# Optimization experiments

Measured on AMD Instinct MI355X. Metric: run time of the kernel, lower is better.

Reference implementation:

```python
import jax, jax.numpy as jnp
import numpy as np

N_NODES = 10000
N_EDGES = 80000
N_GRAPHS = 64
HEADS = 8
F_IN = 128
D1, D2, D3 = 512, 256, 128  # per-head (and output, concat=False) widths
OUT_DIM = 10


def _lin(key, fin, fout):
    kw, kb = jax.random.split(key)
    w = jax.random.normal(kw, (fin, fout), dtype=jnp.float32) * 0.05
    b = jax.random.normal(kb, (fout,), dtype=jnp.float32) * 0.05
    return w, b


def setup_inputs() -> dict:
    key = jax.random.key(0)
    ks = jax.random.split(key, 24)
    x = jax.random.normal(ks[0], (N_NODES, F_IN), dtype=jnp.float32)
    edge_index = jax.random.randint(ks[1], (2, N_EDGES), 0, N_NODES, dtype=jnp.int64)
    batch = jnp.sort(jax.random.randint(ks[2], (N_NODES,), 0, N_GRAPHS, dtype=jnp.int64))
    d = {"x": x, "edge_index": edge_index, "batch": batch}
    # conv1: 128 -> heads*512 (q,k,v), skip 128 -> 512
    d["w_q1"], d["b_q1"] = _lin(ks[3], F_IN, HEADS * D1)
    d["w_k1"], d["b_k1"] = _lin(ks[4], F_IN, HEADS * D1)
    d["w_v1"], d["b_v1"] = _lin(ks[5], F_IN, HEADS * D1)
    d["w_s1"], d["b_s1"] = _lin(ks[6], F_IN, D1)
    # conv2: 512 -> heads*256, skip 512 -> 256
    d["w_q2"], d["b_q2"] = _lin(ks[7], D1, HEADS * D2)
    d["w_k2"], d["b_k2"] = _lin(ks[8], D1, HEADS * D2)
    d["w_v2"], d["b_v2"] = _lin(ks[9], D1, HEADS * D2)
    d["w_s2"], d["b_s2"] = _lin(ks[10], D1, D2)
    # conv3: 256 -> heads*128, skip 256 -> 128
    d["w_q3"], d["b_q3"] = _lin(ks[11], D2, HEADS * D3)
    d["w_k3"], d["b_k3"] = _lin(ks[12], D2, HEADS * D3)
    d["w_v3"], d["b_v3"] = _lin(ks[13], D2, HEADS * D3)
    d["w_s3"], d["b_s3"] = _lin(ks[14], D2, D3)
    # global attention gate + final fc
    d["w_g"], d["b_g"] = _lin(ks[15], D3, 1)
    d["w_fc"], d["b_fc"] = _lin(ks[16], D3, OUT_DIM)
    return d


def _seg_softmax(a, seg, n):
    m = jax.ops.segment_max(a, seg, num_segments=n)
    e = jnp.exp(a - m[seg])
    s = jax.ops.segment_sum(e, seg, num_segments=n)
    return e / (s[seg] + 1e-16)


def _tconv(x, edge_index, wq, bq, wk, bk, wv, bv, ws, bs):
    # PyG TransformerConv, concat=False, root_weight=True, no edge features
    n = x.shape[0]
    c = wq.shape[1] // HEADS
    q = (x @ wq + bq).reshape(n, HEADS, c)
    k = (x @ wk + bk).reshape(n, HEADS, c)
    v = (x @ wv + bv).reshape(n, HEADS, c)
    src, dst = edge_index[0], edge_index[1]
    a = jnp.einsum('ehc,ehc->eh', q[dst], k[src]) / jnp.sqrt(jnp.float32(c))
    alpha = _seg_softmax(a, dst, n)                                  # [E, H]
    out = jax.ops.segment_sum(v[src] * alpha[..., None], dst, num_segments=n)
    return out.mean(axis=1) + (x @ ws + bs)                          # mean over heads + skip


def reference(x, edge_index, batch,
              w_q1, b_q1, w_k1, b_k1, w_v1, b_v1, w_s1, b_s1,
              w_q2, b_q2, w_k2, b_k2, w_v2, b_v2, w_s2, b_s2,
              w_q3, b_q3, w_k3, b_k3, w_v3, b_v3, w_s3, b_s3,
              w_g, b_g, w_fc, b_fc):
    h = jax.nn.elu(_tconv(x, edge_index, w_q1, b_q1, w_k1, b_k1, w_v1, b_v1, w_s1, b_s1))
    h = jax.nn.elu(_tconv(h, edge_index, w_q2, b_q2, w_k2, b_k2, w_v2, b_v2, w_s2, b_s2))
    h = jax.nn.elu(_tconv(h, edge_index, w_q3, b_q3, w_k3, b_k3, w_v3, b_v3, w_s3, b_s3))
    # GlobalAttention pooling: softmax(gate) over nodes within each graph
    gate = h @ w_g + b_g                                             # [N, 1]
    gate = _seg_softmax(gate, batch, N_GRAPHS)
    g = jax.ops.segment_sum(gate * h, batch, num_segments=N_GRAPHS)  # [G, D3]
    return g @ w_fc + b_fc                                           # [G, OUT_DIM]
```

## Files before the change

### kernel.cpp

```cpp
#include <hip/hip_runtime.h>
#include <math.h>

typedef __bf16 bf16;
typedef __bf16 bf16x8 __attribute__((ext_vector_type(8)));
typedef __bf16 bf16x4 __attribute__((ext_vector_type(4)));
typedef __bf16 bf16x2 __attribute__((ext_vector_type(2)));
typedef float f32x4 __attribute__((ext_vector_type(4)));
typedef float f32x2 __attribute__((ext_vector_type(2)));
typedef unsigned int u32;

#define N_NODES 10000
#define N_EDGES 80000
#define N_GRAPHS 64

template<int EPL> struct VecT;
template<> struct VecT<8>{ typedef bf16x8 type; };
template<> struct VecT<4>{ typedef bf16x4 type; };
template<> struct VecT<2>{ typedef bf16x2 type; };

__device__ inline unsigned f2ord(float f){
  unsigned u = __float_as_uint(f);
  return (u & 0x80000000u) ? ~u : (u | 0x80000000u);
}
__device__ inline float ord2f(unsigned u){
  return (u & 0x80000000u) ? __uint_as_float(u & 0x7fffffffu) : __uint_as_float(~u);
}

__device__ inline void gload_lds16(const bf16* g, bf16* l){
  __builtin_amdgcn_global_load_lds(
      (const __attribute__((address_space(1))) unsigned int*)g,
      (__attribute__((address_space(3))) unsigned int*)l, 16, 0, 0);
}

__global__ __launch_bounds__(256) void detect_f32_k(const unsigned short* __restrict__ raw, int n,
                                                    int* __restrict__ flagF){
  int i = blockIdx.x*256 + threadIdx.x;
  if (i < n){
    unsigned e = (raw[i] >> 7) & 0xFFu;
    if (e >= 0xC0u) atomicOr(flagF, 1);
  }
}

struct CvPack {
  const void* src[11];
  bf16* dst[11];
  int pre[12];
  int rl[11];
  int st[11];
};
__global__ __launch_bounds__(256) void convert_all(CvPack p, const int* __restrict__ flagF){
  int gid = blockIdx.x*256 + threadIdx.x;
  if (gid >= p.pre[11]) return;
  int t = 0;
  while (gid >= p.pre[t+1]) ++t;
  int i = gid - p.pre[t];
  bool f = (*flagF != 0);
  float v = f ? ((const float*)p.src[t])[i] : (float)((const bf16*)p.src[t])[i];
  int row = i / p.rl[t], col = i - row*p.rl[t];
  p.dst[t][(size_t)row*p.st[t] + col] = (bf16)v;
}

__global__ __launch_bounds__(256) void detect_i64(const int* __restrict__ raw, int* __restrict__ flag){
  int i = blockIdx.x*256 + threadIdx.x;
  if (i < 4000 && raw[2*i+1] != 0) atomicOr(flag, 1);
}

__global__ __launch_bounds__(256) void conv_idx(const int* __restrict__ ei_raw,
                                                const int* __restrict__ b_raw,
                                                const int* __restrict__ flag,
                                                int* __restrict__ src, int* __restrict__ dst,
                                                int* __restrict__ bat, int* __restrict__ cnt){
  int i = blockIdx.x*256 + threadIdx.x;
  bool i32 = (*flag != 0);
  if (i < N_EDGES){
    int s = i32 ? ei_raw[i]   : ei_raw[2*i];
    int d = i32 ? ei_raw[N_EDGES + i] : ei_raw[2*(N_EDGES + i)];
    s = min(max(s, 0), N_NODES-1);
    d = min(max(d, 0), N_NODES-1);
    src[i] = s; dst[i] = d;
    atomicAdd(&cnt[d], 1);
  }
  if (i < N_NODES){
    int b = i32 ? b_raw[i] : b_raw[2*i];
    bat[i] = min(max(b, 0), N_GRAPHS-1);
  }
}

__global__ __launch_bounds__(256) void scanA(const int* __restrict__ cnt, int* __restrict__ fill,
                                             int* __restrict__ bsum, int N){
  __shared__ int s[256];
  int i = blockIdx.x*256 + threadIdx.x;
  int v = (i < N) ? cnt[i] : 0;
  s[threadIdx.x] = v;
  __syncthreads();
  for (int d = 1; d < 256; d <<= 1){
    int t = (threadIdx.x >= d) ? s[threadIdx.x - d] : 0;
    __syncthreads();
    s[threadIdx.x] += t;
    __syncthreads();
  }
  if (i < N) fill[i] = s[threadIdx.x] - v;
  if (threadIdx.x == 255) bsum[blockIdx.x] = s[255];
}
__global__ __launch_bounds__(64) void scanB(int* __restrict__ bsum, int nb){
  if (threadIdx.x == 0){
    int a = 0;
    for (int b = 0; b < nb; ++b){ int t = bsum[b]; bsum[b] = a; a += t; }
  }
}
__global__ __launch_bounds__(256) void scanC(const int* __restrict__ bsum, int* __restrict__ fill,
                                             int* __restrict__ row_ptr, int N){
  int i = blockIdx.x*256 + threadIdx.x;
  if (i < N){
    int st = fill[i] + bsum[i >> 8];
    fill[i] = st;
    row_ptr[i] = st;
  }
  if (i == 0) row_ptr[N] = N_EDGES;
}

__global__ __launch_bounds__(256) void fill_csr(const int* __restrict__ dst,
                                                int* __restrict__ fill, int* __restrict__ eids){
  int e = blockIdx.x*256 + threadIdx.x;
  if (e < N_EDGES){
    int p = atomicAdd(&fill[dst[e]], 1);
    eids[p] = e;
  }
}

__global__ __launch_bounds__(256)
void gemm_bias(const bf16* __restrict__ A, int lda,
               const bf16* __restrict__ Bt,
               const bf16* __restrict__ bias, bf16* __restrict__ Cout, int ldc,
               int M, int N, int K)
{
  __shared__ bf16 As[128*64];
  __shared__ bf16 Bs[128*64];
  const int tid = threadIdx.x;
  const int lane = tid & 63;
  const int wave = tid >> 6;
  const int m0 = blockIdx.y * 128, n0 = blockIdx.x * 128;
  const int wm = (wave >> 1) * 64, wn = (wave & 1) * 64;
  const int l15 = lane & 15, l4 = lane >> 4;
  const int srow = lane >> 3;
  const int schunk = lane & 7;

  f32x4 acc[4][4] = {};

  for (int k0 = 0; k0 < K; k0 += 64){
    #pragma unroll
    for (int j = 0; j < 4; ++j){
      int r0 = (wave*4 + j)*8;
      int r  = r0 + srow;
      int gc = schunk ^ (r & 7);
      int ga = m0 + r; if (ga >= M) ga = M-1;
      gload_lds16(A  + (size_t)ga*lda      + k0 + gc*8, As + r0*64);
      gload_lds16(Bt + (size_t)(n0 + r)*K  + k0 + gc*8, Bs + r0*64);
    }
    __syncthreads();
    #pragma unroll
    for (int kt = 0; kt < 2; ++kt){
      bf16x8 af[4], bfr[4];
      #pragma unroll
      for (int mt = 0; mt < 4; ++mt){
        int row = wm + mt*16 + l15;
        int p = (kt*4 + l4) ^ (l15 & 7);
        af[mt] = *(const bf16x8*)(As + row*64 + p*8);
      }
      #pragma unroll
      for (int nt = 0; nt < 4; ++nt){
        int row = wn + nt*16 + l15;
        int p = (kt*4 + l4) ^ (l15 & 7);
        bfr[nt] = *(const bf16x8*)(Bs + row*64 + p*8);
      }
      #pragma unroll
      for (int mt = 0; mt < 4; ++mt)
        #pragma unroll
        for (int nt = 0; nt < 4; ++nt)
          acc[mt][nt] = __builtin_amdgcn_mfma_f32_16x16x32_bf16(af[mt], bfr[nt], acc[mt][nt], 0, 0, 0);
    }
    __syncthreads();
  }

  #pragma unroll
  for (int nt = 0; nt < 4; ++nt){
    int col = n0 + wn + nt*16 + l15;
    float bv = (float)bias[col];
    #pragma unroll
    for (int mt = 0; mt < 4; ++mt){
      int rbase = m0 + wm + mt*16 + l4*4;
      #pragma unroll
      for (int r = 0; r < 4; ++r){
        int row = rbase + r;
        if (row < M) Cout[(size_t)row*ldc + col] = (bf16)(acc[mt][nt][r] + bv);
      }
    }
  }
}

__global__ __launch_bounds__(512, 1)
void gemm8p_bias(const bf16* __restrict__ A, int lda,
                 const bf16* __restrict__ Bt,
                 const bf16* __restrict__ bias, bf16* __restrict__ Cout, int ldc,
                 int M, int K)
{
  __shared__ bf16 As[3][256*64];
  __shared__ bf16 Bs[3][128*64];
  const int tid = threadIdx.x;
  const int lane = tid & 63;
  const int wave = tid >> 6;
  const int m0 = blockIdx.y * 256, n0 = blockIdx.x * 128;
  const int wm = (wave >> 1) * 64;
  const int wn = (wave & 1) * 64;
  const int l15 = lane & 15, l4 = lane >> 4;
  const int srow = lane >> 3;
  const int schunk = lane & 7;
  const int NT = K >> 6;

  auto stageA = [&](int t, int j){
    int b = t % 3;
    int r0 = (wave + j*8)*8;
    int r  = r0 + srow;
    int gc = schunk ^ srow;
    int ga = m0 + r; if (ga >= M) ga = M-1;
    gload_lds16(A + (size_t)ga*lda + t*64 + gc*8, &As[b][r0*64]);
  };
  auto stageB = [&](int t, int j){
    int b = t % 3;
    int r0 = (wave + j*8)*8;
    int r  = r0 + srow;
    int gc = schunk ^ srow;
    gload_lds16(Bt + (size_t)(n0 + r)*K + t*64 + gc*8, &Bs[b][r0*64]);
  };

  stageA(0,0); stageA(0,1); stageA(0,2); stageA(0,3); stageB(0,0); stageB(0,1);
  if (NT > 1){ stageA(1,0); stageA(1,1); stageA(1,2); stageA(1,3); stageB(1,0); stageB(1,1); }
  if (NT > 1) asm volatile("s_waitcnt vmcnt(6)" ::: "memory");
  else        asm volatile("s_waitcnt vmcnt(0)" ::: "memory");
  __builtin_amdgcn_s_barrier();

  f32x4 acc[4][4] = {};

  for (int t = 0; t < NT; ++t){
    const bf16* as = &As[t % 3][0];
    const bf16* bs = &Bs[t % 3][0];
    bf16x8 bfr[4][2];
    bf16x8 af[2][2];

    #pragma unroll
    for (int nt2 = 0; nt2 < 4; ++nt2)
      #pragma unroll
      for (int kt = 0; kt < 2; ++kt){
        int row = wn + nt2*16 + l15;
        int p = (kt*4 + l4) ^ (l15 & 7);
        bfr[nt2][kt] = *(const bf16x8*)(bs + row*64 + p*8);
      }
    #pragma unroll
    for (int i = 0; i < 2; ++i)
      #pragma unroll
      for (int kt = 0; kt < 2; ++kt){
        int row = wm + i*16 + l15;
        int p = (kt*4 + l4) ^ (l15 & 7);
        af[i][kt] = *(const bf16x8*)(as + row*64 + p*8);
      }
    if (t + 2 < NT){ stageA(t+2,0); stageA(t+2,1); stageB(t+2,0); }
    __builtin_amdgcn_s_setprio(1);
    #pragma unroll
    for (int i = 0; i < 2; ++i)
      #pragma unroll
      for (int nt2 = 0; nt2 < 4; ++nt2)
        #pragma unroll
        for (int kt = 0; kt < 2; ++kt)
          acc[i][nt2] = __builtin_amdgcn_mfma_f32_16x16x32_bf16(af[i][kt], bfr[nt2][kt], acc[i][nt2], 0, 0, 0);
    __builtin_amdgcn_s_setprio(0);

    #pragma unroll
    for (int i = 0; i < 2; ++i)
      #pragma unroll
      for (int kt = 0; kt < 2; ++kt){
        int row = wm + (2+i)*16 + l15;
        int p = (kt*4 + l4) ^ (l15 & 7);
        af[i][kt] = *(const bf16x8*)(as + row*64 + p*8);
      }
    if (t + 2 < NT){ stageA(t+2,2); stageA(t+2,3); stageB(t+2,1); }
    __builtin_amdgcn_s_setprio(1);
    #pragma unroll
    for (int i = 0; i < 2; ++i)
      #pragma unroll
      for (int nt2 = 0; nt2 < 4; ++nt2)
        #pragma unroll
        for (int kt = 0; kt < 2; ++kt)
          acc[2+i][nt2] = __builtin_amdgcn_mfma_f32_16x16x32_bf16(af[i][kt], bfr[nt2][kt], acc[2+i][nt2], 0, 0, 0);
    __builtin_amdgcn_s_setprio(0);

    if (t < NT - 1){
      if (t + 2 < NT) asm volatile("s_waitcnt vmcnt(6)" ::: "memory");
      else            asm volatile("s_waitcnt vmcnt(0)" ::: "memory");
      __builtin_amdgcn_s_barrier();
    }
  }

  #pragma unroll
  for (int nt2 = 0; nt2 < 4; ++nt2){
    int col = n0 + wn + nt2*16 + l15;
    float bv = (float)bias[col];
    #pragma unroll
    for (int mt = 0; mt < 4; ++mt){
      int rbase = m0 + wm + mt*16 + l4*4;
      #pragma unroll
      for (int r = 0; r < 4; ++r){
        int row = rbase + r;
        if (row < M) Cout[(size_t)row*ldc + col] = (bf16)(acc[mt][nt2][r] + bv);
      }
    }
  }
}

template<int BM, int OUTMODE>
__global__ __launch_bounds__(256)
void gemm_fused(const bf16* __restrict__ A, int lda,
                const bf16* __restrict__ Bt,
                const bf16* __restrict__ bp, const bf16* __restrict__ mb,
                const int* __restrict__ row_ptr,
                bf16* __restrict__ outB, int ldo, float* __restrict__ outF,
                int M, int K)
{
  constexpr int PA    = BM/32;
  constexpr int WCOLS = 128/BM;
  constexpr int WTN   = BM;
  constexpr int NT    = WTN/16;
  __shared__ bf16 As[BM*64];
  __shared__ bf16 Bs[128*64];
  const int tid = threadIdx.x;
  const int lane = tid & 63;
  const int wave = tid >> 6;
  const int m0 = blockIdx.y * BM, n0 = blockIdx.x * 128;
  const int wm = (wave / WCOLS) * 32;
  const int wn = (wave % WCOLS) * WTN;
  const int l15 = lane & 15, l4 = lane >> 4;
  const int srow = lane >> 3;
  const int schunk = lane & 7;

  f32x4 acc[2][NT] = {};

  for (int k0 = 0; k0 < K; k0 += 64){
    #pragma unroll
    for (int j = 0; j < PA; ++j){
      int r0 = (wave*PA + j)*8;
      int r  = r0 + srow;
      int gc = schunk ^ (r & 7);
      int ga = m0 + r; if (ga >= M) ga = M-1;
      gload_lds16(A + (size_t)ga*lda + k0 + gc*8, As + r0*64);
    }
    #pragma unroll
    for (int j = 0; j < 4; ++j){
      int r0 = (wave*4 + j)*8;
      int r  = r0 + srow;
      int gc = schunk ^ (r & 7);
      gload_lds16(Bt + (size_t)(n0 + r)*K + k0 + gc*8, Bs + r0*64);
    }
    __syncthreads();
    #pragma unroll
    for (int kt = 0; kt < 2; ++kt){
      bf16x8 af[2], bfr[NT];
      #pragma unroll
      for (int mt = 0; mt < 2; ++mt){
        int row = wm + mt*16 + l15;
        int p = (kt*4 + l4) ^ (l15 & 7);
        af[mt] = *(const bf16x8*)(As + row*64 + p*8);
      }
      #pragma unroll
      for (int nt = 0; nt < NT; ++nt){
        int row = wn + nt*16 + l15;
        int p = (kt*4 + l4) ^ (l15 & 7);
        bfr[nt] = *(const bf16x8*)(Bs + row*64 + p*8);
      }
      #pragma unroll
      for (int mt = 0; mt < 2; ++mt)
        #pragma unroll
        for (int nt = 0; nt < NT; ++nt)
          acc[mt][nt] = __builtin_amdgcn_mfma_f32_16x16x32_bf16(af[mt], bfr[nt], acc[mt][nt], 0, 0, 0);
    }
    __syncthreads();
  }

  if (OUTMODE == 0){
    float bv[NT], mv[NT];
    #pragma unroll
    for (int nt = 0; nt < NT; ++nt){
      int col = n0 + wn + nt*16 + l15;
      bv[nt] = (float)bp[col];
      mv[nt] = (float)mb[col];
    }
    #pragma unroll
    for (int mt = 0; mt < 2; ++mt){
      int rbase = m0 + wm + mt*16 + l4*4;
      #pragma unroll
      for (int r = 0; r < 4; ++r){
        int row = rbase + r;
        if (row < M){
          bool d0 = (row_ptr[row+1] == row_ptr[row]);
          #pragma unroll
          for (int nt = 0; nt < NT; ++nt){
            int col = n0 + wn + nt*16 + l15;
            float v = acc[mt][nt][r] + bv[nt] - (d0 ? mv[nt] : 0.f);
            v = (v > 0.f) ? v : (__expf(v) - 1.f);
            outB[(size_t)row*ldo + col] = (bf16)v;
          }
        }
      }
    }
  } else {
    #pragma unroll
    for (int mt = 0; mt < 2; ++mt){
      int rbase = m0 + wm + mt*16 + l4*4;
      #pragma unroll
      for (int r = 0; r < 4; ++r){
        int row = rbase + r;
        if (row < M){
          #pragma unroll
          for (int nt = 0; nt < NT; ++nt){
            int col = n0 + wn + nt*16 + l15;
            outF[(size_t)row*128 + col] = acc[mt][nt][r];
          }
        }
      }
    }
  }
}

__global__ __launch_bounds__(256)
void finalize_gate(const float* __restrict__ facc, const bf16* __restrict__ bp,
                   const bf16* __restrict__ mb, const int* __restrict__ row_ptr,
                   bf16* __restrict__ hout, const bf16* __restrict__ wg,
                   const bf16* __restrict__ bg, const int* __restrict__ bat,
                   float* __restrict__ gate, unsigned* __restrict__ gmax)
{
  __shared__ float wred[4];
  int idx = blockIdx.x*256 + threadIdx.x;
  int n = idx >> 7, c = idx & 127;
  bool d0 = (row_ptr[n+1] == row_ptr[n]);
  float v = facc[idx] + (float)bp[c] - (d0 ? (float)mb[c] : 0.f);
  v = (v > 0.f) ? v : (__expf(v) - 1.f);
  hout[idx] = (bf16)v;
  float gc = v * (float)wg[c];
  #pragma unroll
  for (int o = 32; o; o >>= 1) gc += __shfl_xor(gc, o, 64);
  int wave = threadIdx.x >> 6;
  if ((threadIdx.x & 63) == 0) wred[wave] = gc;
  __syncthreads();
  if ((threadIdx.x & 127) == 0){
    float g = wred[wave] + wred[wave + 1] + (float)bg[0];
    gate[n] = g;
    atomicMax(&gmax[bat[n]], f2ord(g));
  }
}

struct MhPack { const bf16* wk[3]; const bf16* wq[3]; bf16* wzt[3]; int fin[3]; int c[3]; };
__global__ __launch_bounds__(256)
void gemm_mh_all(MhPack P)
{
  const int L = blockIdx.z >> 3, h = blockIdx.z & 7;
  const int Fin = P.fin[L], C = P.c[L];
  const int nb = Fin >> 7;
  if ((int)blockIdx.x >= nb || (int)blockIdx.y >= nb) return;
  __shared__ bf16 As[128*64];
  __shared__ bf16 Bs[128*64];
  const int ld = 8*C;
  const bf16* Ab = P.wk[L] + h*C;
  const bf16* Bb = P.wq[L] + h*C;
  bf16* Cb = P.wzt[L] + (size_t)h*Fin*Fin;
  const int tid = threadIdx.x;
  const int lane = tid & 63;
  const int wave = tid >> 6;
  const int m0 = blockIdx.y * 128, n0 = blockIdx.x * 128;
  const int wm = (wave >> 1) * 64, wn = (wave & 1) * 64;
  const int l15 = lane & 15, l4 = lane >> 4;
  const int srow = lane >> 3;
  const int schunk = lane & 7;

  f32x4 acc[4][4] = {};

  for (int k0 = 0; k0 < C; k0 += 64){
    #pragma unroll
    for (int j = 0; j < 4; ++j){
      int r0 = (wave*4 + j)*8;
      int r  = r0 + srow;
      int gc = schunk ^ (r & 7);
      gload_lds16(Ab + (size_t)(m0 + r)*ld + k0 + gc*8, As + r0*64);
      gload_lds16(Bb + (size_t)(n0 + r)*ld + k0 + gc*8, Bs + r0*64);
    }
    __syncthreads();
    #pragma unroll
    for (int kt = 0; kt < 2; ++kt){
      bf16x8 af[4], bfr[4];
      #pragma unroll
      for (int mt = 0; mt < 4; ++mt){
        int row = wm + mt*16 + l15;
        int p = (kt*4 + l4) ^ (l15 & 7);
        af[mt] = *(const bf16x8*)(As + row*64 + p*8);
      }
      #pragma unroll
      for (int nt = 0; nt < 4; ++nt){
        int row = wn + nt*16 + l15;
        int p = (kt*4 + l4) ^ (l15 & 7);
        bfr[nt] = *(const bf16x8*)(Bs + row*64 + p*8);
      }
      #pragma unroll
      for (int mt = 0; mt < 4; ++mt)
        #pragma unroll
        for (int nt = 0; nt < 4; ++nt)
          acc[mt][nt] = __builtin_amdgcn_mfma_f32_16x16x32_bf16(af[mt], bfr[nt], acc[mt][nt], 0, 0, 0);
    }
    __syncthreads();
  }

  #pragma unroll
  for (int nt = 0; nt < 4; ++nt){
    int col = n0 + wn + nt*16 + l15;
    #pragma unroll
    for (int mt = 0; mt < 4; ++mt){
      int rbase = m0 + wm + mt*16 + l4*4;
      #pragma unroll
      for (int r = 0; r < 4; ++r)
        Cb[(size_t)(rbase + r)*Fin + col] = (bf16)acc[mt][nt][r];
    }
  }
}

struct WvPack { const void* wv[3]; const void* ws[3]; bf16* bt[3]; int fin[3]; int c[3]; int bx[3]; int by[3]; };
__global__ __launch_bounds__(256)
void prep_wv_all(WvPack P, const int* __restrict__ flagF)
{
  const int L = blockIdx.z;
  if ((int)blockIdx.x >= P.bx[L] || (int)blockIdx.y >= P.by[L]) return;
  __shared__ float t[32][33];
  bool f = (*flagF != 0);
  const int Fin = P.fin[L], C = P.c[L];
  int k0 = blockIdx.x*32, j0 = blockIdx.y*32;
  int x = threadIdx.x & 31, y = threadIdx.x >> 5;
  const void* srcp; int nstride, cb; float sc; int i0;
  if (k0 < 8*Fin){
    int h = k0 / Fin; i0 = k0 - h*Fin;
    srcp = P.wv[L]; nstride = 8*C; cb = h*C + j0; sc = 0.125f;
  } else {
    i0 = k0 - 8*Fin;
    srcp = P.ws[L]; nstride = C; cb = j0; sc = 1.0f;
  }
  #pragma unroll
  for (int ii = 0; ii < 4; ++ii){
    int i = i0 + y + ii*8;
    size_t idx = (size_t)i*nstride + cb + x;
    float v = f ? ((const float*)srcp)[idx] : (float)((const bf16*)srcp)[idx];
    t[y + ii*8][x] = v*sc;
  }
  __syncthreads();
  #pragma unroll
  for (int ii = 0; ii < 4; ++ii){
    int j = j0 + y + ii*8;
    P.bt[L][(size_t)j*(9*Fin) + k0 + x] = (bf16)t[x][y + ii*8];
  }
}

struct SmPack { const bf16* wkc[3]; const void* bq[3]; const void* bv[3]; const void* bs[3];
                int fin[3]; int c[3]; bf16* tz[3]; bf16* bp[3]; bf16* mb[3]; int rb[3]; int bpb[3]; };
__global__ __launch_bounds__(256)
void prep_small_all(SmPack P, const int* __restrict__ flagF)
{
  const int L = blockIdx.z;
  const int Fin = P.fin[L], C = P.c[L];
  const int rb = P.rb[L];
  if ((int)blockIdx.x >= rb + P.bpb[L]) return;
  bool f = (*flagF != 0);
  if ((int)blockIdx.x < rb){
    int wave = threadIdx.x >> 6, lane = threadIdx.x & 63;
    int r = blockIdx.x*4 + wave;
    int h = r / Fin, i = r - h*Fin;
    int epc = C >> 6;
    const bf16* wp = P.wkc[L] + (size_t)i*8*C + h*C;
    const void* bqp = P.bq[L];
    float s = 0.f;
    for (int k = 0; k < epc; ++k){
      int c = k*64 + lane;
      float b = f ? ((const float*)bqp)[h*C + c] : (float)((const bf16*)bqp)[h*C + c];
      s += (float)wp[c] * b;
    }
    #pragma unroll
    for (int o = 32; o; o >>= 1) s += __shfl_xor(s, o, 64);
    if (lane == 0) P.tz[L][r] = (bf16)s;
  } else {
    int idx = ((int)blockIdx.x - rb)*256 + threadIdx.x;
    if (idx < C){
      float s = 0.f;
      for (int h = 0; h < 8; ++h)
        s += f ? ((const float*)P.bv[L])[h*C + idx] : (float)((const bf16*)P.bv[L])[h*C + idx];
      s *= 0.125f;
      float bsv = f ? ((const float*)P.bs[L])[idx] : (float)((const bf16*)P.bs[L])[idx];
      P.mb[L][idx] = (bf16)s;
      P.bp[L][idx] = (bf16)(s + bsv);
    }
  }
}

template<int Fin, int NHT>
__global__ __launch_bounds__(256)
void node_edge(const bf16* __restrict__ z, int zw, int hbase,
               bf16* __restrict__ AP, int ldP,
               const int* __restrict__ row_ptr, const int* __restrict__ eids,
               const int* __restrict__ srcv, float scale)
{
  constexpr int EPL  = Fin/64;
  constexpr int EPL2 = EPL/2;
  constexpr int KC   = Fin/32;
  typedef typename VecT<EPL>::type vecb;
  __shared__ float sw[4][68][12];

  const int wave = threadIdx.x >> 6;
  const int lane = threadIdx.x & 63;
  const int n = blockIdx.x*4 + wave;

  const int beg = row_ptr[n];
  int deg = row_ptr[n+1] - beg;
  if (deg > 64) deg = 64;

  bf16* APn = AP + (size_t)n*ldP;

  if (deg == 0){
    vecb zv;
    #pragma unroll
    for (int k = 0; k < EPL; ++k) zv[k] = (bf16)0.f;
    #pragma unroll
    for (int h = 0; h < NHT; ++h)
      *(vecb*)(APn + (size_t)(hbase + h)*Fin + lane*EPL) = zv;
    return;
  }

  int e_ld = (lane < deg) ? lane : 0;
  int srcReg = srcv[eids[beg + e_ld]];

  const int nc = (deg + 15) >> 4;
  const int l15 = lane & 15, l4 = lane >> 4;
  const int h   = l15 & (NHT-1);
  const bf16* zp = z + (size_t)n*zw + (size_t)h*Fin + l4*8;

  f32x4 sacc[4];
  #pragma unroll
  for (int c = 0; c < 4; ++c) sacc[c] = (f32x4){0.f,0.f,0.f,0.f};

  #pragma unroll
  for (int c = 0; c < 4; ++c){
    if (c < nc){
      int sn = __shfl(srcReg, c*16 + l15, 64);
      const bf16* ap = AP + (size_t)sn*ldP + 8*Fin + l4*8;
      f32x4 s = (f32x4){0.f,0.f,0.f,0.f};
      #pragma unroll
      for (int k = 0; k < KC; ++k){
        bf16x8 af = *(const bf16x8*)(ap + k*32);
        bf16x8 bv = *(const bf16x8*)(zp + k*32);
        s = __builtin_amdgcn_mfma_f32_16x16x32_bf16(af, bv, s, 0, 0, 0);
      }
      sacc[c] = s;
    }
  }

  float m = -3.4e38f;
  #pragma unroll
  for (int c = 0; c < 4; ++c){
    if (c < nc){
      #pragma unroll
      for (int r = 0; r < 4; ++r){
        int row = c*16 + l4*4 + r;
        float v = sacc[c][r]*scale;
        sacc[c][r] = v;
        if (row < deg) m = fmaxf(m, v);
      }
    }
  }
  m = fmaxf(m, __shfl_xor(m, 16, 64));
  m = fmaxf(m, __shfl_xor(m, 32, 64));
  float ssum = 0.f;
  #pragma unroll
  for (int c = 0; c < 4; ++c){
    if (c < nc){
      #pragma unroll
      for (int r = 0; r < 4; ++r){
        int row = c*16 + l4*4 + r;
        float e = (row < deg) ? __expf(sacc[c][r] - m) : 0.f;
        sacc[c][r] = e;
        ssum += e;
      }
    }
  }
  ssum += __shfl_xor(ssum, 16, 64);
  ssum += __shfl_xor(ssum, 32, 64);
  float inv = 1.f/(ssum + 1e-16f);

  if (l15 < NHT){
    #pragma unroll
    for (int c = 0; c < 4; ++c){
      if (c < nc){
        #pragma unroll
        for (int r = 0; r < 4; ++r)
          sw[wave][c*16 + l4*4 + r][l15] = sacc[c][r]*inv;
      }
    }
  }
  if (lane < 4*NHT)
    sw[wave][nc*16 + (lane >> 3)][lane & 7] = 0.f;

  f32x2 acc[NHT][EPL2];
  #pragma unroll
  for (int hh = 0; hh < NHT; ++hh)
    #pragma unroll
    for (int p = 0; p < EPL2; ++p) acc[hh][p] = (f32x2){0.f,0.f};

  for (int i0 = 0; i0 < deg; i0 += 4){
    int sn0 = __shfl(srcReg, i0,   64);
    int sn1 = __shfl(srcReg, i0+1, 64);
    int sn2 = __shfl(srcReg, i0+2, 64);
    int sn3 = __shfl(srcReg, i0+3, 64);
    vecb hv0 = *(const vecb*)(AP + (size_t)sn0*ldP + 8*Fin + lane*EPL);
    vecb hv1 = *(const vecb*)(AP + (size_t)sn1*ldP + 8*Fin + lane*EPL);
    vecb hv2 = *(const vecb*)(AP + (size_t)sn2*ldP + 8*Fin + lane*EPL);
    vecb hv3 = *(const vecb*)(AP + (size_t)sn3*ldP + 8*Fin + lane*EPL);
    #pragma unroll
    for (int j = 0; j < 4; ++j){
      int e = i0 + j;
      vecb hv = (j == 0) ? hv0 : (j == 1) ? hv1 : (j == 2) ? hv2 : hv3;
      f32x4 w0 = *(const f32x4*)&sw[wave][e][0];
      f32x4 w1 = (NHT == 8) ? *(const f32x4*)&sw[wave][e][4] : w0;
      f32x2 xf[EPL2];
      const u32* up = (const u32*)&hv;
      #pragma unroll
      for (int p = 0; p < EPL2; ++p){
        u32 u = up[p];
        xf[p] = (f32x2){ __uint_as_float(u << 16), __uint_as_float(u & 0xffff0000u) };
      }
      #pragma unroll
      for (int hh = 0; hh < NHT; ++hh){
        float w = (hh < 4) ? w0[hh] : w1[hh-4];
        f32x2 wv = (f32x2){w, w};
        #pragma unroll
        for (int p = 0; p < EPL2; ++p)
          acc[hh][p] += wv * xf[p];
      }
    }
  }

  #pragma unroll
  for (int hh = 0; hh < NHT; ++hh){
    vecb o;
    #pragma unroll
    for (int p = 0; p < EPL2; ++p){
      o[2*p]   = (bf16)acc[hh][p][0];
      o[2*p+1] = (bf16)acc[hh][p][1];
    }
    *(vecb*)(APn + (size_t)(hbase + hh)*Fin + lane*EPL) = o;
  }
}

__global__ __launch_bounds__(256) void gate_expsum(float* __restrict__ gate, const int* __restrict__ bat,
                                                   const unsigned* __restrict__ gmax, float* __restrict__ gsum){
  int n = blockIdx.x*256 + threadIdx.x;
  if (n < N_NODES){
    float e = __expf(gate[n] - ord2f(gmax[bat[n]]));
    gate[n] = e;
    atomicAdd(&gsum[bat[n]], e);
  }
}

__global__ __launch_bounds__(256) void pool_weighted(const float* __restrict__ gate, const float* __restrict__ gsum,
                                                     const int* __restrict__ bat, const bf16* __restrict__ h,
                                                     float* __restrict__ gacc){
  int n = blockIdx.x*4 + (threadIdx.x >> 6);
  if (n >= N_NODES) return;
  int lane = threadIdx.x & 63;
  int b = bat[n];
  float w = gate[n]/(gsum[b] + 1e-16f);
  atomicAdd(&gacc[b*128 + lane],      w*(float)h[(size_t)n*128 + lane]);
  atomicAdd(&gacc[b*128 + 64 + lane], w*(float)h[(size_t)n*128 + 64 + lane]);
}

__global__ __launch_bounds__(64) void final_fc(const float* __restrict__ gacc, const bf16* __restrict__ wfc,
                                               const bf16* __restrict__ bfc, void* __restrict__ out,
                                               const int* __restrict__ flagF){
  int g = blockIdx.x;
  int o = threadIdx.x;
  if (o < 10){
    float s = (float)bfc[o];
    for (int c = 0; c < 128; ++c) s += gacc[g*128 + c]*(float)wfc[c*10 + o];
    if (*flagF) ((float*)out)[(size_t)g*10 + o] = s;
    else        ((bf16*)out)[(size_t)g*10 + o]  = (bf16)s;
  }
}

extern "C" void kernel_launch(void* const* d_in, const int* in_sizes, int n_in,
                              void* d_out, int out_size, void* d_ws, size_t ws_size,
                              hipStream_t stream)
{
  const int* ei   = (const int*)d_in[1];
  const int* braw = (const int*)d_in[2];

  bf16 *Wzt1=0,*Wzt2=0,*Wzt3=0,*Wvt1=0,*Wvt2=0,*Wvt3=0;
  float *facc=0,*gate=0;
  bf16 *tz1=0,*tz2=0,*tz3=0,*bp1=0,*mb1=0,*bp2=0,*mb2=0,*bp3=0,*mb3=0,*h3=0;
  bf16 *cwg=0,*cbg=0,*cwfc=0,*cbfc=0;
  int *src=0,*dst=0,*bat=0,*cnt=0,*row_ptr=0,*fillp=0,*eids=0,*flagbuf=0;
  char *A1=0, *A2=0;

  auto plan = [&](bool big)->size_t{
    size_t off = 0;
    auto A = [&](size_t bytes)->char*{
      char* p = (char*)d_ws + off;
      off += (bytes + 255) & ~(size_t)255;
      return p;
    };
    A1 = A(92160000);
    A2 = A(big ? 81920000 : 46080000);
    Wzt1 = (bf16*)A((size_t)8*128*128*2);
    Wzt2 = (bf16*)A((size_t)8*512*512*2);
    Wzt3 = (bf16*)A((size_t)8*256*256*2);
    Wvt1 = (bf16*)A((size_t)512*9*128*2);
    Wvt2 = (bf16*)A((size_t)256*9*512*2);
    Wvt3 = (bf16*)A((size_t)128*9*256*2);
    facc = (float*)A((size_t)N_NODES*512*4);
    tz1  = (bf16*)A(8*128*2);
    tz2  = (bf16*)A(8*512*2);
    tz3  = (bf16*)A(8*256*2);
    bp1  = (bf16*)A(512*2);  mb1 = (bf16*)A(512*2);
    bp2  = (bf16*)A(256*2);  mb2 = (bf16*)A(256*2);
    bp3  = (bf16*)A(128*2);  mb3 = (bf16*)A(128*2);
    h3   = (bf16*)A((size_t)N_NODES*128*2);
    src  = (int*)A((size_t)N_EDGES*4);
    dst  = (int*)A((size_t)N_EDGES*4);
    bat  = (int*)A((size_t)N_NODES*4);
    cnt  = (int*)A((size_t)N_NODES*4);
    row_ptr = (int*)A((size_t)(N_NODES+1)*4);
    fillp= (int*)A((size_t)N_NODES*4);
    eids = (int*)A((size_t)N_EDGES*4);
    flagbuf = (int*)A(16384);
    gate = (float*)A((size_t)N_NODES*4);
    unsigned* poolz = (unsigned*)A((size_t)(64 + 64 + 64*128)*4);
    (void)poolz;
    cwg  = (bf16*)A(128*2);
    cbg  = (bf16*)A(2*2);
    cwfc = (bf16*)A(1280*2);
    cbfc = (bf16*)A(10*2);
    return off;
  };

  bool big = (plan(true) <= ws_size);
  if (!big && plan(false) > ws_size) return;
  plan(big);
  unsigned* poolz = (unsigned*)((char*)gate + (((size_t)N_NODES*4 + 255) & ~(size_t)255));

  int* flagI = flagbuf;
  int* flagF = flagbuf + 1;
  int* bsum  = (int*)((char*)flagbuf + 8192);
  unsigned* gmax = poolz;
  float*    gsum = (float*)(poolz + 64);
  float*    gacc = (float*)(poolz + 128);

  bf16* AP1 = (bf16*)A2;   const int ldP1 = 1152;
  bf16* z1  = (bf16*)A1;
  bf16* AP2 = (bf16*)A1;   const int ldP2 = 4608;
  bf16* z2  = (bf16*)A2;
  bf16* AP3 = (bf16*)A2;   const int ldP3 = 2304;
  bf16* z3  = (bf16*)A1;
  bf16* wq1c = (bf16*)(A1 + 48000000);  bf16* wk1c = wq1c + 128*4096;
  bf16* wq2c = wk1c + 128*4096;         bf16* wk2c = wq2c + 512*2048;
  bf16* wq3c = wk2c + 512*2048;         bf16* wk3c = wq3c + 256*1024;

  hipMemsetAsync(flagbuf, 0, 16384, stream);
  {
    int nprobe = in_sizes[0] < 32768 ? in_sizes[0] : 32768;
    detect_f32_k<<<(nprobe + 255)/256, 256, 0, stream>>>((const unsigned short*)d_in[0], nprobe, flagF);
    detect_i64<<<16, 256, 0, stream>>>(ei, flagI);
  }

  {
    CvPack p;
    const int CIDX[11] = {0, 3, 5, 11, 13, 19, 21, 27, 28, 29, 30};
    bf16* CDST[11] = {AP1 + 1024, wq1c, wk1c, wq2c, wk2c, wq3c, wk3c, cwg, cbg, cwfc, cbfc};
    int tot = 0;
    for (int t = 0; t < 11; ++t){
      p.src[t] = d_in[CIDX[t]];
      p.dst[t] = CDST[t];
      p.pre[t] = tot;
      int n = in_sizes[CIDX[t]];
      tot += n;
      if (t == 0){ p.rl[t] = 128; p.st[t] = 1152; }
      else       { p.rl[t] = n;   p.st[t] = n;    }
    }
    p.pre[11] = tot;
    convert_all<<<(tot + 255)/256, 256, 0, stream>>>(p, flagF);
  }

  hipMemsetAsync(cnt, 0, (size_t)N_NODES*4, stream);
  conv_idx<<<(N_EDGES + 255)/256, 256, 0, stream>>>(ei, braw, flagI, src, dst, bat, cnt);
  scanA<<<40, 256, 0, stream>>>(cnt, fillp, bsum, N_NODES);
  scanB<<<1, 64, 0, stream>>>(bsum, 40);
  scanC<<<40, 256, 0, stream>>>(bsum, fillp, row_ptr, N_NODES);
  fill_csr<<<(N_EDGES + 255)/256, 256, 0, stream>>>(dst, fillp, eids);

  {
    MhPack mp;
    mp.wk[0]=wk1c; mp.wk[1]=wk2c; mp.wk[2]=wk3c;
    mp.wq[0]=wq1c; mp.wq[1]=wq2c; mp.wq[2]=wq3c;
    mp.wzt[0]=Wzt1; mp.wzt[1]=Wzt2; mp.wzt[2]=Wzt3;
    mp.fin[0]=128; mp.fin[1]=512; mp.fin[2]=256;
    mp.c[0]=512; mp.c[1]=256; mp.c[2]=128;
    gemm_mh_all<<<dim3(4,4,24), 256, 0, stream>>>(mp);

    WvPack wp;
    wp.wv[0]=d_in[7];  wp.wv[1]=d_in[15]; wp.wv[2]=d_in[23];
    wp.ws[0]=d_in[9];  wp.ws[1]=d_in[17]; wp.ws[2]=d_in[25];
    wp.bt[0]=Wvt1; wp.bt[1]=Wvt2; wp.bt[2]=Wvt3;
    wp.fin[0]=128; wp.fin[1]=512; wp.fin[2]=256;
    wp.c[0]=512; wp.c[1]=256; wp.c[2]=128;
    wp.bx[0]=36; wp.bx[1]=144; wp.bx[2]=72;
    wp.by[0]=16; wp.by[1]=8;   wp.by[2]=4;
    prep_wv_all<<<dim3(144,16,3), 256, 0, stream>>>(wp, flagF);

    SmPack sp;
    sp.wkc[0]=wk1c; sp.wkc[1]=wk2c; sp.wkc[2]=wk3c;
    sp.bq[0]=d_in[4];  sp.bq[1]=d_in[12]; sp.bq[2]=d_in[20];
    sp.bv[0]=d_in[8];  sp.bv[1]=d_in[16]; sp.bv[2]=d_in[24];
    sp.bs[0]=d_in[10]; sp.bs[1]=d_in[18]; sp.bs[2]=d_in[26];
    sp.fin[0]=128; sp.fin[1]=512; sp.fin[2]=256;
    sp.c[0]=512; sp.c[1]=256; sp.c[2]=128;
    sp.tz[0]=tz1; sp.tz[1]=tz2; sp.tz[2]=tz3;
    sp.bp[0]=bp1; sp.bp[1]=bp2; sp.bp[2]=bp3;
    sp.mb[0]=mb1; sp.mb[1]=mb2; sp.mb[2]=mb3;
    sp.rb[0]=256;  sp.rb[1]=1024; sp.rb[2]=512;
    sp.bpb[0]=2;   sp.bpb[1]=1;   sp.bpb[2]=1;
    prep_small_all<<<dim3(1025,1,3), 256, 0, stream>>>(sp, flagF);
  }

  const int MT = (N_NODES + 127)/128;
  const int NB = N_NODES/4;
  const int MT32 = (N_NODES + 31)/32;
  const int MT64 = (N_NODES + 63)/64;
  const int MT256 = (N_NODES + 255)/256;
  const float sc1 = 1.0f/sqrtf(512.f), sc2 = 1.0f/sqrtf(256.f), sc3 = 1.0f/sqrtf(128.f);

  hipMemsetAsync(poolz, 0, (size_t)(64 + 64 + 64*128)*4, stream);

  gemm_bias<<<dim3(8, MT), 256, 0, stream>>>(AP1 + 1024, ldP1, Wzt1, tz1, z1, 1024, N_NODES, 1024, 128);
  node_edge<128,8><<<NB, 256, 0, stream>>>(z1, 1024, 0, AP1, ldP1, row_ptr, eids, src, sc1);
  gemm_fused<64,0><<<dim3(4, MT64), 256, 0, stream>>>(AP1, ldP1, Wvt1, bp1, mb1, row_ptr,
                                                      AP2 + 4096, ldP2, (float*)0, N_NODES, 1152);

  if (big){
    gemm8p_bias<<<dim3(32, MT256), 512, 0, stream>>>(AP2 + 4096, ldP2, Wzt2, tz2, z2, 4096, N_NODES, 512);
    node_edge<512,8><<<NB, 256, 0, stream>>>(z2, 4096, 0, AP2, ldP2, row_ptr, eids, src, sc2);
  } else {
    for (int g = 0; g < 2; ++g){
      gemm_bias<<<dim3(16, MT), 256, 0, stream>>>(AP2 + 4096, ldP2, Wzt2 + (size_t)g*4*512*512, tz2 + g*4*512, z2, 2048, N_NODES, 2048, 512);
      node_edge<512,4><<<NB, 256, 0, stream>>>(z2, 2048, g*4, AP2, ldP2, row_ptr, eids, src, sc2);
    }
  }
  gemm_fused<32,0><<<dim3(2, MT32), 256, 0, stream>>>(AP2, ldP2, Wvt2, bp2, mb2, row_ptr,
                                                      AP3 + 2048, ldP3, (float*)0, N_NODES, 4608);

  gemm8p_bias<<<dim3(16, MT256), 512, 0, stream>>>(AP3 + 2048, ldP3, Wzt3, tz3, z3, 2048, N_NODES, 256);
  node_edge<256,8><<<NB, 256, 0, stream>>>(z3, 2048, 0, AP3, ldP3, row_ptr, eids, src, sc3);
  gemm_fused<32,1><<<dim3(1, MT32), 256, 0, stream>>>(AP3, ldP3, Wvt3, (const bf16*)0, (const bf16*)0, (const int*)0,
                                                      (bf16*)0, 0, facc, N_NODES, 2304);
  finalize_gate<<<(N_NODES*128)/256, 256, 0, stream>>>(facc, bp3, mb3, row_ptr, h3, cwg, cbg, bat, gate, gmax);

  gate_expsum<<<(N_NODES + 255)/256, 256, 0, stream>>>(gate, bat, gmax, gsum);
  pool_weighted<<<(N_NODES + 3)/4, 256, 0, stream>>>(gate, gsum, bat, h3, gacc);
  final_fc<<<N_GRAPHS, 64, 0, stream>>>(gacc, cwfc, cbfc, d_out, flagF);
}
```

Baseline: 652.3 us.

## Replace atomic gate softmax pooling with per-graph block reduction over sorted batch

```diff
diff --git a/kernel.cpp b/kernel.cpp
--- a/kernel.cpp
+++ b/kernel.cpp
@@ -17,14 +17,6 @@
 template<> struct VecT<8>{ typedef bf16x8 type; };
 template<> struct VecT<4>{ typedef bf16x4 type; };
 template<> struct VecT<2>{ typedef bf16x2 type; };
-
-__device__ inline unsigned f2ord(float f){
-  unsigned u = __float_as_uint(f);
-  return (u & 0x80000000u) ? ~u : (u | 0x80000000u);
-}
-__device__ inline float ord2f(unsigned u){
-  return (u & 0x80000000u) ? __uint_as_float(u & 0x7fffffffu) : __uint_as_float(~u);
-}
 
 __device__ inline void gload_lds16(const bf16* g, bf16* l){
   __builtin_amdgcn_global_load_lds(
@@ -433,8 +425,7 @@
 void finalize_gate(const float* __restrict__ facc, const bf16* __restrict__ bp,
                    const bf16* __restrict__ mb, const int* __restrict__ row_ptr,
                    bf16* __restrict__ hout, const bf16* __restrict__ wg,
-                   const bf16* __restrict__ bg, const int* __restrict__ bat,
-                   float* __restrict__ gate, unsigned* __restrict__ gmax)
+                   const bf16* __restrict__ bg, float* __restrict__ gate)
 {
   __shared__ float wred[4];
   int idx = blockIdx.x*256 + threadIdx.x;
@@ -452,7 +443,48 @@
   if ((threadIdx.x & 127) == 0){
     float g = wred[wave] + wred[wave + 1] + (float)bg[0];
     gate[n] = g;
-    atomicMax(&gmax[bat[n]], f2ord(g));
+  }
+}
+
+__global__ __launch_bounds__(256)
+void pool_graphs(const float* __restrict__ gate, const int* __restrict__ bat,
+                 const bf16* __restrict__ h, float* __restrict__ gacc)
+{
+  int b = blockIdx.x;
+  int lo = 0, hi = N_NODES;
+  while (lo < hi){ int mid = (lo + hi) >> 1; if (bat[mid] < b) lo = mid + 1; else hi = mid; }
+  int s = lo;
+  lo = s; hi = N_NODES;
+  while (lo < hi){ int mid = (lo + hi) >> 1; if (bat[mid] < b + 1) lo = mid + 1; else hi = mid; }
+  int e = lo;
+
+  int t = threadIdx.x;
+  float m = -3.4e38f;
+  for (int n = s + t; n < e; n += 256) m = fmaxf(m, gate[n]);
+  #pragma unroll
+  for (int o = 32; o; o >>= 1) m = fmaxf(m, __shfl_xor(m, o, 64));
+  __shared__ float red[4];
+  int wv = t >> 6;
+  if ((t & 63) == 0) red[wv] = m;
+  __syncthreads();
+  m = fmaxf(fmaxf(red[0], red[1]), fmaxf(red[2], red[3]));
+
+  int team = t >> 7, c = t & 127;
+  float acc = 0.f, se = 0.f;
+  for (int n = s + team; n < e; n += 2){
+    float en = __expf(gate[n] - m);
+    acc += en * (float)h[(size_t)n*128 + c];
+    if (c == 0) se += en;
+  }
+  __shared__ float accs[256];
+  __shared__ float ses[2];
+  accs[t] = acc;
+  if (c == 0) ses[team] = se;
+  __syncthreads();
+  if (t < 128){
+    float tot = accs[t] + accs[128 + t];
+    float S = ses[0] + ses[1];
+    gacc[b*128 + t] = tot / (S + 1e-16f);
   }
 }
 
@@ -757,28 +789,6 @@
     }
     *(vecb*)(APn + (size_t)(hbase + hh)*Fin + lane*EPL) = o;
   }
-}
-
-__global__ __launch_bounds__(256) void gate_expsum(float* __restrict__ gate, const int* __restrict__ bat,
-                                                   const unsigned* __restrict__ gmax, float* __restrict__ gsum){
-  int n = blockIdx.x*256 + threadIdx.x;
-  if (n < N_NODES){
-    float e = __expf(gate[n] - ord2f(gmax[bat[n]]));
-    gate[n] = e;
-    atomicAdd(&gsum[bat[n]], e);
-  }
-}
-
-__global__ __launch_bounds__(256) void pool_weighted(const float* __restrict__ gate, const float* __restrict__ gsum,
-                                                     const int* __restrict__ bat, const bf16* __restrict__ h,
-                                                     float* __restrict__ gacc){
-  int n = blockIdx.x*4 + (threadIdx.x >> 6);
-  if (n >= N_NODES) return;
-  int lane = threadIdx.x & 63;
-  int b = bat[n];
-  float w = gate[n]/(gsum[b] + 1e-16f);
-  atomicAdd(&gacc[b*128 + lane],      w*(float)h[(size_t)n*128 + lane]);
-  atomicAdd(&gacc[b*128 + 64 + lane], w*(float)h[(size_t)n*128 + 64 + lane]);
 }
 
 __global__ __launch_bounds__(64) void final_fc(const float* __restrict__ gacc, const bf16* __restrict__ wfc,
@@ -857,8 +867,6 @@
   int* flagI = flagbuf;
   int* flagF = flagbuf + 1;
   int* bsum  = (int*)((char*)flagbuf + 8192);
-  unsigned* gmax = poolz;
-  float*    gsum = (float*)(poolz + 64);
   float*    gacc = (float*)(poolz + 128);
 
   bf16* AP1 = (bf16*)A2;   const int ldP1 = 1152;
@@ -944,8 +952,6 @@
   const int MT256 = (N_NODES + 255)/256;
   const float sc1 = 1.0f/sqrtf(512.f), sc2 = 1.0f/sqrtf(256.f), sc3 = 1.0f/sqrtf(128.f);
 
-  hipMemsetAsync(poolz, 0, (size_t)(64 + 64 + 64*128)*4, stream);
-
   gemm_bias<<<dim3(8, MT), 256, 0, stream>>>(AP1 + 1024, ldP1, Wzt1, tz1, z1, 1024, N_NODES, 1024, 128);
   node_edge<128,8><<<NB, 256, 0, stream>>>(z1, 1024, 0, AP1, ldP1, row_ptr, eids, src, sc1);
   gemm_fused<64,0><<<dim3(4, MT64), 256, 0, stream>>>(AP1, ldP1, Wvt1, bp1, mb1, row_ptr,
@@ -967,9 +973,8 @@
   node_edge<256,8><<<NB, 256, 0, stream>>>(z3, 2048, 0, AP3, ldP3, row_ptr, eids, src, sc3);
   gemm_fused<32,1><<<dim3(1, MT32), 256, 0, stream>>>(AP3, ldP3, Wvt3, (const bf16*)0, (const bf16*)0, (const int*)0,
                                                       (bf16*)0, 0, facc, N_NODES, 2304);
-  finalize_gate<<<(N_NODES*128)/256, 256, 0, stream>>>(facc, bp3, mb3, row_ptr, h3, cwg, cbg, bat, gate, gmax);
-
-  gate_expsum<<<(N_NODES + 255)/256, 256, 0, stream>>>(gate, bat, gmax, gsum);
-  pool_weighted<<<(N_NODES + 3)/4, 256, 0, stream>>>(gate, gsum, bat, h3, gacc);
+  finalize_gate<<<(N_NODES*128)/256, 256, 0, stream>>>(facc, bp3, mb3, row_ptr, h3, cwg, cbg, gate);
+
+  pool_graphs<<<N_GRAPHS, 256, 0, stream>>>(gate, bat, h3, gacc);
   final_fc<<<N_GRAPHS, 64, 0, stream>>>(gacc, cwfc, cbfc, d_out, flagF);
 }
```

After: 554.7 us. 15.0% less time.
